# Kernel tuning notes

Hardware: AMD Instinct MI355X
Metric: run time of the kernel (lower is better)

The kernel has to match this reference:

```python
import jax, jax.numpy as jnp
import numpy as np

B, NB, BD, H = 524288, 8, 16, 64  # batch, n_bundles, bundle_dim, hidden_dim

def setup_inputs() -> dict:
    key = jax.random.key(0)
    ks = jax.random.split(key, 8)
    z = jax.random.normal(ks[0], (B, NB, BD), dtype=jnp.float32)
    w1 = jax.random.normal(ks[1], (H, NB), dtype=jnp.float32) * (1.0 / np.sqrt(NB))
    b1 = jnp.zeros((H,), dtype=jnp.float32)
    w2 = jax.random.normal(ks[2], (H, H), dtype=jnp.float32) * (1.0 / np.sqrt(H))
    b2 = jnp.zeros((H,), dtype=jnp.float32)
    w3 = jax.random.normal(ks[3], (NB, H), dtype=jnp.float32) * (1.0 / np.sqrt(H))
    mix_w = jax.random.normal(ks[4], (NB, NB, BD, BD), dtype=jnp.float32) * 0.01
    gate_bias = jnp.zeros((NB,), dtype=jnp.float32)
    return {"z": z, "w1": w1, "b1": b1, "w2": w2, "b2": b2, "w3": w3,
            "mix_w": mix_w, "gate_bias": gate_bias}

def reference(z, w1, b1, w2, b2, w3, mix_w, gate_bias):
    # per-bundle norms: [B, NB]
    norms = jnp.linalg.norm(z, axis=-1) + 1e-8
    # tiny gating MLP (exact GELU like torch nn.GELU default)
    h = jax.nn.gelu(norms @ w1.T + b1, approximate=False)
    h = jax.nn.gelu(h @ w2.T + b2, approximate=False)
    scales = jax.nn.softplus(h @ w3.T)                      # [B, NB]
    equivariant = z * scales[:, :, None]                    # [B, NB, BD]
    # cross-bundle mixing: mixing[b,i,k] = sum_{j,d} z[b,j,d] * W[i,j,k,d]
    mixing = jnp.einsum('bjd,ijkd->bik', z, mix_w)          # [B, NB, BD]
    gates = jax.nn.sigmoid(gate_bias)[None, :, None]        # [1, NB, 1]
    return z + (equivariant + gates * mixing)
```

## Files before the change

kernel.cpp:

```cpp
#include <hip/hip_runtime.h>
#include <hip/hip_fp16.h>

typedef __bf16   bf16x8 __attribute__((ext_vector_type(8)));
typedef _Float16 f16x8  __attribute__((ext_vector_type(8)));
typedef float    f32x4  __attribute__((ext_vector_type(4)));
typedef unsigned short ushort8 __attribute__((ext_vector_type(8)));

__device__ __forceinline__ unsigned short f2bf(float f){
  unsigned u = __builtin_bit_cast(unsigned, f);
  u = (u + 0x7FFFu + ((u >> 16) & 1u)) >> 16;
  return (unsigned short)u;
}

__device__ __forceinline__ float gelu_fast(float x){
  float u = 0.7978845608f * x * __builtin_fmaf(0.044715f, x * x, 1.0f);
  float e = __expf(2.0f * __builtin_fabsf(u));
  float t = __builtin_fmaf(-2.0f, __builtin_amdgcn_rcpf(e + 1.0f), 1.0f);
  t = __builtin_copysignf(t, u);
  return 0.5f * x * (1.0f + t);
}

__device__ __forceinline__ float softplus_fast(float x){
  float e = __expf(-__builtin_fabsf(x));
  return fmaxf(x, 0.0f) + __logf(1.0f + e);
}

__global__ void prepack_wt(const float* __restrict__ mix_w,
                           unsigned short* __restrict__ wt){
  int tid = blockIdx.x * 256 + threadIdx.x;
  int f = tid >> 6, L = tid & 63;
  int ks = f & 3, nt = f >> 2;
  int q = L >> 4, c = L & 15;
  int N = nt * 16 + c;
  int i = N >> 4, ko = N & 15;
  unsigned pk[4];
#pragma unroll
  for (int p = 0; p < 4; ++p){
    int K0 = ks * 32 + q * 8 + 2 * p;
    int K1 = K0 + 1;
    unsigned lo = f2bf(mix_w[((i*8 + (K0>>4))*16 + ko)*16 + (K0&15)]);
    unsigned hi = f2bf(mix_w[((i*8 + (K1>>4))*16 + ko)*16 + (K1&15)]);
    pk[p] = lo | (hi << 16);
  }
  uint4 v; v.x = pk[0]; v.y = pk[1]; v.z = pk[2]; v.w = pk[3];
  ((uint4*)wt)[tid] = v;
}

__global__ __launch_bounds__(256, 5)
void soft_eq_kernel(const float* __restrict__ z,
                    const float* __restrict__ w1,  const float* __restrict__ b1,
                    const float* __restrict__ w2,  const float* __restrict__ b2,
                    const float* __restrict__ w3,  const float* __restrict__ gate_bias,
                    const unsigned short* __restrict__ wt,
                    float* __restrict__ out){
  __shared__ __align__(16) _Float16 h1s[64 * 64];
  __shared__ __align__(16) _Float16 h2s[64 * 64];
  __shared__ float gatesS[8];
  float (*normsS)[8] = (float(*)[8])h2s;
  float (*scalesS)[9] = (float(*)[9])h1s;

  const int t = threadIdx.x;
  const size_t base = (size_t)blockIdx.x * (64 * 128);
  const float4* zg = (const float4*)(z + base);

#pragma unroll
  for (int it = 0; it < 8; ++it){
    int idx = t + it * 256;
    float4 v = zg[idx];
    int r  = idx >> 5;
    int bi = (idx & 31) >> 2;
    float ss = v.x*v.x + v.y*v.y + v.z*v.z + v.w*v.w;
    ss += __shfl_xor(ss, 1);
    ss += __shfl_xor(ss, 2);
    if ((t & 3) == 0) normsS[r][bi] = sqrtf(ss) + 1e-8f;
  }

  const int i = t & 63, rg = t >> 6;
  float w1r[8];
  { const float4* p = (const float4*)(w1 + i * 8);
    float4 a = p[0], bq = p[1];
    w1r[0]=a.x; w1r[1]=a.y; w1r[2]=a.z; w1r[3]=a.w;
    w1r[4]=bq.x; w1r[5]=bq.y; w1r[6]=bq.z; w1r[7]=bq.w; }
  const float b1r = b1[i];
  __syncthreads();

#pragma unroll
  for (int chunk = 0; chunk < 16; ++chunk){
    int r = chunk * 4 + rg;
    const float4* np = (const float4*)normsS[r];
    float4 n0 = np[0], n1 = np[1];
    float pre = b1r + n0.x*w1r[0] + n0.y*w1r[1] + n0.z*w1r[2] + n0.w*w1r[3]
                    + n1.x*w1r[4] + n1.y*w1r[5] + n1.z*w1r[6] + n1.w*w1r[7];
    int u = (i >> 3) ^ (r & 7);
    h1s[r * 64 + u * 8 + (i & 7)] = (_Float16)gelu_fast(pre);
  }
  __syncthreads();

  const int w = rg, L = t & 63, q = L >> 4, c = L & 15;
  const int am = w * 16 + c;

  f16x8 a2[2];
#pragma unroll
  for (int ks = 0; ks < 2; ++ks){
    int u = (ks * 4 + q) ^ (am & 7);
    a2[ks] = *(const f16x8*)&h1s[am * 64 + u * 8];
  }
#pragma unroll
  for (int nt = 0; nt < 4; ++nt){
    int n = nt * 16 + c;
    f32x4 acc2 = {};
#pragma unroll
    for (int ks = 0; ks < 2; ++ks){
      const float4* wp = (const float4*)(w2 + n * 64 + ks * 32 + q * 8);
      float4 v0 = wp[0], v1 = wp[1];
      f16x8 bf;
      bf[0]=(_Float16)v0.x; bf[1]=(_Float16)v0.y; bf[2]=(_Float16)v0.z; bf[3]=(_Float16)v0.w;
      bf[4]=(_Float16)v1.x; bf[5]=(_Float16)v1.y; bf[6]=(_Float16)v1.z; bf[7]=(_Float16)v1.w;
      acc2 = __builtin_amdgcn_mfma_f32_16x16x32_f16(a2[ks], bf, acc2, 0, 0, 0);
    }
    float b2v = b2[n];
#pragma unroll
    for (int rr = 0; rr < 4; ++rr){
      int row = w * 16 + q * 4 + rr;
      int uu = (n >> 3) ^ (row & 7);
      h2s[row * 64 + uu * 8 + (n & 7)] = (_Float16)gelu_fast(acc2[rr] + b2v);
    }
  }
  __syncthreads();

  {
    f16x8 a3[2];
#pragma unroll
    for (int ks = 0; ks < 2; ++ks){
      int u = (ks * 4 + q) ^ (am & 7);
      a3[ks] = *(const f16x8*)&h2s[am * 64 + u * 8];
    }
    int n3 = c & 7;
    f32x4 acc3 = {};
#pragma unroll
    for (int ks = 0; ks < 2; ++ks){
      const float4* wp = (const float4*)(w3 + n3 * 64 + ks * 32 + q * 8);
      float4 v0 = wp[0], v1 = wp[1];
      f16x8 bf;
      bf[0]=(_Float16)v0.x; bf[1]=(_Float16)v0.y; bf[2]=(_Float16)v0.z; bf[3]=(_Float16)v0.w;
      bf[4]=(_Float16)v1.x; bf[5]=(_Float16)v1.y; bf[6]=(_Float16)v1.z; bf[7]=(_Float16)v1.w;
      acc3 = __builtin_amdgcn_mfma_f32_16x16x32_f16(a3[ks], bf, acc3, 0, 0, 0);
    }
    if (c < 8){
#pragma unroll
      for (int rr = 0; rr < 4; ++rr){
        int row = w * 16 + q * 4 + rr;
        scalesS[row][c] = softplus_fast(acc3[rr]);
      }
    }
  }
  if (t < 8) gatesS[t] = __builtin_amdgcn_rcpf(1.0f + __expf(-gate_bias[t]));
  __syncthreads();

  f32x4 acc[8] = {};
  const uint4* wtf = (const uint4*)wt;
  const float* zp = z + base;
#pragma unroll
  for (int ks = 0; ks < 4; ++ks){
    int ak = ks * 32 + q * 8;
    const float4* ap = (const float4*)(zp + am * 128 + ak);
    float4 a0 = ap[0], a1 = ap[1];
    ushort8 au;
    au[0]=f2bf(a0.x); au[1]=f2bf(a0.y); au[2]=f2bf(a0.z); au[3]=f2bf(a0.w);
    au[4]=f2bf(a1.x); au[5]=f2bf(a1.y); au[6]=f2bf(a1.z); au[7]=f2bf(a1.w);
    bf16x8 af = __builtin_bit_cast(bf16x8, au);
#pragma unroll
    for (int n = 0; n < 8; ++n){
      uint4 bv = wtf[(n * 4 + ks) * 64 + L];
      bf16x8 bfr = __builtin_bit_cast(bf16x8, bv);
      acc[n] = __builtin_amdgcn_mfma_f32_16x16x32_bf16(af, bfr, acc[n], 0, 0, 0);
    }
  }

  float* op = out + base;
#pragma unroll
  for (int n = 0; n < 8; ++n){
    float gate = gatesS[n];
#pragma unroll
    for (int rr = 0; rr < 4; ++rr){
      int row = w * 16 + q * 4 + rr;
      int col = n * 16 + c;
      float zv = zp[row * 128 + col];
      float sc = scalesS[row][n];
      op[row * 128 + col] = __builtin_fmaf(zv, sc, __builtin_fmaf(gate, acc[n][rr], zv));
    }
  }
}

extern "C" void kernel_launch(void* const* d_in, const int* in_sizes, int n_in,
                              void* d_out, int out_size, void* d_ws, size_t ws_size,
                              hipStream_t stream){
  const float* z         = (const float*)d_in[0];
  const float* w1        = (const float*)d_in[1];
  const float* b1        = (const float*)d_in[2];
  const float* w2        = (const float*)d_in[3];
  const float* b2        = (const float*)d_in[4];
  const float* w3        = (const float*)d_in[5];
  const float* mix_w     = (const float*)d_in[6];
  const float* gate_bias = (const float*)d_in[7];
  float* out = (float*)d_out;
  unsigned short* wt = (unsigned short*)d_ws;

  int B = in_sizes[0] / 128;
  prepack_wt<<<8, 256, 0, stream>>>(mix_w, wt);
  soft_eq_kernel<<<B / 64, 256, 0, stream>>>(z, w1, b1, w2, b2, w3, gate_bias, wt, out);
}
```

Measured before the change: 575.7 us.

## Load z once into registers, stage output via LDS for coalesced stores, prepack MLP weights

Each thread now loads its z row fragment into registers once and reuses it for both the norm computation and the bf16 mixing MFMA, which is moved ahead of the gating MLP. The epilogue stages gate*mixing through LDS in two halves so that z re-reads and output writes become row-contiguous float4 accesses. A new prepack kernel converts w2 and w3 to fp16 in MFMA fragment layout, removing per-block conversion. The cost is higher register pressure (launch bounds lowered to 4 waves), extra barriers, and one more small launch.

```diff
diff --git a/kernel.cpp b/kernel.cpp
--- a/kernel.cpp
+++ b/kernel.cpp
@@ -24,6 +24,7 @@
   float e = __expf(-__builtin_fabsf(x));
   return fmaxf(x, 0.0f) + __logf(1.0f + e);
 }
+
 
 __global__ void prepack_wt(const float* __restrict__ mix_w,
                            unsigned short* __restrict__ wt){
@@ -46,48 +47,96 @@
   ((uint4*)wt)[tid] = v;
 }
 
-__global__ __launch_bounds__(256, 5)
+__global__ void prepack_mlp(const float* __restrict__ w2,
+                            const float* __restrict__ w3,
+                            unsigned short* __restrict__ ws){
+  int tid = blockIdx.x * 256 + threadIdx.x;
+  if (tid < 512){
+    int f = tid >> 6, L = tid & 63;
+    int nt = f >> 1, ks = f & 1, q = L >> 4, c = L & 15;
+    const float* s = w2 + (nt*16 + c)*64 + ks*32 + q*8;
+    f16x8 h;
+#pragma unroll
+    for (int j = 0; j < 8; ++j) h[j] = (_Float16)s[j];
+    ((f16x8*)(ws + 16384))[tid] = h;
+  } else if (tid < 640){
+    int u = tid - 512;
+    int ks = u >> 6, L = u & 63, q = L >> 4, c = L & 15;
+    const float* s = w3 + (c & 7)*64 + ks*32 + q*8;
+    f16x8 h;
+#pragma unroll
+    for (int j = 0; j < 8; ++j) h[j] = (_Float16)s[j];
+    ((f16x8*)(ws + 20480))[u] = h;
+  }
+}
+
+__global__ __launch_bounds__(256, 4)
 void soft_eq_kernel(const float* __restrict__ z,
                     const float* __restrict__ w1,  const float* __restrict__ b1,
                     const float* __restrict__ w2,  const float* __restrict__ b2,
                     const float* __restrict__ w3,  const float* __restrict__ gate_bias,
                     const unsigned short* __restrict__ wt,
                     float* __restrict__ out){
-  __shared__ __align__(16) _Float16 h1s[64 * 64];
-  __shared__ __align__(16) _Float16 h2s[64 * 64];
-  __shared__ float gatesS[8];
-  float (*normsS)[8] = (float(*)[8])h2s;
-  float (*scalesS)[9] = (float(*)[9])h1s;
+  __shared__ __align__(16) unsigned char smemU[17408 + 3104];
+  _Float16* h1s = (_Float16*)smemU;
+  _Float16* h2s = (_Float16*)(smemU + 8192);
+  float*    stageF = (float*)smemU;
+  float*    nsS = (float*)(smemU + 17408);
 
   const int t = threadIdx.x;
+  const int w = t >> 6, L = t & 63, q = L >> 4, c = L & 15;
   const size_t base = (size_t)blockIdx.x * (64 * 128);
-  const float4* zg = (const float4*)(z + base);
-
-#pragma unroll
-  for (int it = 0; it < 8; ++it){
-    int idx = t + it * 256;
-    float4 v = zg[idx];
-    int r  = idx >> 5;
-    int bi = (idx & 31) >> 2;
-    float ss = v.x*v.x + v.y*v.y + v.z*v.z + v.w*v.w;
-    ss += __shfl_xor(ss, 1);
-    ss += __shfl_xor(ss, 2);
-    if ((t & 3) == 0) normsS[r][bi] = sqrtf(ss) + 1e-8f;
-  }
-
-  const int i = t & 63, rg = t >> 6;
+  const float* zp = z + base;
+
+  const int zrow = w * 16 + c;
+  const float* zr0 = zp + zrow * 128;
+  float4 zr[8];
+#pragma unroll
+  for (int ks = 0; ks < 4; ++ks){
+    zr[2*ks]   = *(const float4*)(zr0 + ks*32 + q*8);
+    zr[2*ks+1] = *(const float4*)(zr0 + ks*32 + q*8 + 4);
+  }
+#pragma unroll
+  for (int ks = 0; ks < 4; ++ks){
+    float4 a = zr[2*ks], b = zr[2*ks+1];
+    float ss = a.x*a.x + a.y*a.y + a.z*a.z + a.w*a.w
+             + b.x*b.x + b.y*b.y + b.z*b.z + b.w*b.w;
+    ss += __shfl_xor(ss, 16);
+    if (!(L & 16))
+      nsS[zrow * 12 + 2*ks + (q >> 1)] = sqrtf(ss) + 1e-8f;
+  }
+
+  const int i = t & 63;
   float w1r[8];
   { const float4* p = (const float4*)(w1 + i * 8);
     float4 a = p[0], bq = p[1];
     w1r[0]=a.x; w1r[1]=a.y; w1r[2]=a.z; w1r[3]=a.w;
     w1r[4]=bq.x; w1r[5]=bq.y; w1r[6]=bq.z; w1r[7]=bq.w; }
   const float b1r = b1[i];
+
+  f32x4 acc[8] = {};
+  const uint4* wtf = (const uint4*)wt;
+#pragma unroll
+  for (int ks = 0; ks < 4; ++ks){
+    float4 a0 = zr[2*ks], a1 = zr[2*ks+1];
+    ushort8 au;
+    au[0]=f2bf(a0.x); au[1]=f2bf(a0.y); au[2]=f2bf(a0.z); au[3]=f2bf(a0.w);
+    au[4]=f2bf(a1.x); au[5]=f2bf(a1.y); au[6]=f2bf(a1.z); au[7]=f2bf(a1.w);
+    bf16x8 af = __builtin_bit_cast(bf16x8, au);
+#pragma unroll
+    for (int n = 0; n < 8; ++n){
+      uint4 bv = wtf[(n * 4 + ks) * 64 + L];
+      bf16x8 bfr = __builtin_bit_cast(bf16x8, bv);
+      acc[n] = __builtin_amdgcn_mfma_f32_16x16x32_bf16(af, bfr, acc[n], 0, 0, 0);
+    }
+  }
+
   __syncthreads();
 
 #pragma unroll
   for (int chunk = 0; chunk < 16; ++chunk){
-    int r = chunk * 4 + rg;
-    const float4* np = (const float4*)normsS[r];
+    int r = chunk * 4 + w;
+    const float4* np = (const float4*)&nsS[r * 12];
     float4 n0 = np[0], n1 = np[1];
     float pre = b1r + n0.x*w1r[0] + n0.y*w1r[1] + n0.z*w1r[2] + n0.w*w1r[3]
                     + n1.x*w1r[4] + n1.y*w1r[5] + n1.z*w1r[6] + n1.w*w1r[7];
@@ -96,9 +145,9 @@
   }
   __syncthreads();
 
-  const int w = rg, L = t & 63, q = L >> 4, c = L & 15;
   const int am = w * 16 + c;
 
+  const f16x8* w2f = (const f16x8*)(wt + 16384);
   f16x8 a2[2];
 #pragma unroll
   for (int ks = 0; ks < 2; ++ks){
@@ -110,14 +159,9 @@
     int n = nt * 16 + c;
     f32x4 acc2 = {};
 #pragma unroll
-    for (int ks = 0; ks < 2; ++ks){
-      const float4* wp = (const float4*)(w2 + n * 64 + ks * 32 + q * 8);
-      float4 v0 = wp[0], v1 = wp[1];
-      f16x8 bf;
-      bf[0]=(_Float16)v0.x; bf[1]=(_Float16)v0.y; bf[2]=(_Float16)v0.z; bf[3]=(_Float16)v0.w;
-      bf[4]=(_Float16)v1.x; bf[5]=(_Float16)v1.y; bf[6]=(_Float16)v1.z; bf[7]=(_Float16)v1.w;
-      acc2 = __builtin_amdgcn_mfma_f32_16x16x32_f16(a2[ks], bf, acc2, 0, 0, 0);
-    }
+    for (int ks = 0; ks < 2; ++ks)
+      acc2 = __builtin_amdgcn_mfma_f32_16x16x32_f16(a2[ks], w2f[(nt*2+ks)*64 + L],
+                                                    acc2, 0, 0, 0);
     float b2v = b2[n];
 #pragma unroll
     for (int rr = 0; rr < 4; ++rr){
@@ -129,66 +173,60 @@
   __syncthreads();
 
   {
+    const f16x8* w3f = (const f16x8*)(wt + 20480);
     f16x8 a3[2];
 #pragma unroll
     for (int ks = 0; ks < 2; ++ks){
       int u = (ks * 4 + q) ^ (am & 7);
       a3[ks] = *(const f16x8*)&h2s[am * 64 + u * 8];
     }
-    int n3 = c & 7;
     f32x4 acc3 = {};
 #pragma unroll
-    for (int ks = 0; ks < 2; ++ks){
-      const float4* wp = (const float4*)(w3 + n3 * 64 + ks * 32 + q * 8);
-      float4 v0 = wp[0], v1 = wp[1];
-      f16x8 bf;
-      bf[0]=(_Float16)v0.x; bf[1]=(_Float16)v0.y; bf[2]=(_Float16)v0.z; bf[3]=(_Float16)v0.w;
-      bf[4]=(_Float16)v1.x; bf[5]=(_Float16)v1.y; bf[6]=(_Float16)v1.z; bf[7]=(_Float16)v1.w;
-      acc3 = __builtin_amdgcn_mfma_f32_16x16x32_f16(a3[ks], bf, acc3, 0, 0, 0);
-    }
+    for (int ks = 0; ks < 2; ++ks)
+      acc3 = __builtin_amdgcn_mfma_f32_16x16x32_f16(a3[ks], w3f[ks*64 + L],
+                                                    acc3, 0, 0, 0);
     if (c < 8){
 #pragma unroll
       for (int rr = 0; rr < 4; ++rr){
         int row = w * 16 + q * 4 + rr;
-        scalesS[row][c] = softplus_fast(acc3[rr]);
+        nsS[row * 12 + c] = softplus_fast(acc3[rr]);
       }
     }
   }
-  if (t < 8) gatesS[t] = __builtin_amdgcn_rcpf(1.0f + __expf(-gate_bias[t]));
-  __syncthreads();
-
-  f32x4 acc[8] = {};
-  const uint4* wtf = (const uint4*)wt;
-  const float* zp = z + base;
-#pragma unroll
-  for (int ks = 0; ks < 4; ++ks){
-    int ak = ks * 32 + q * 8;
-    const float4* ap = (const float4*)(zp + am * 128 + ak);
-    float4 a0 = ap[0], a1 = ap[1];
-    ushort8 au;
-    au[0]=f2bf(a0.x); au[1]=f2bf(a0.y); au[2]=f2bf(a0.z); au[3]=f2bf(a0.w);
-    au[4]=f2bf(a1.x); au[5]=f2bf(a1.y); au[6]=f2bf(a1.z); au[7]=f2bf(a1.w);
-    bf16x8 af = __builtin_bit_cast(bf16x8, au);
-#pragma unroll
-    for (int n = 0; n < 8; ++n){
-      uint4 bv = wtf[(n * 4 + ks) * 64 + L];
-      bf16x8 bfr = __builtin_bit_cast(bf16x8, bv);
-      acc[n] = __builtin_amdgcn_mfma_f32_16x16x32_bf16(af, bfr, acc[n], 0, 0, 0);
-    }
-  }
+  if (t < 8) nsS[768 + t] = __builtin_amdgcn_rcpf(1.0f + __expf(-gate_bias[t]));
+  __syncthreads();
 
   float* op = out + base;
 #pragma unroll
-  for (int n = 0; n < 8; ++n){
-    float gate = gatesS[n];
-#pragma unroll
-    for (int rr = 0; rr < 4; ++rr){
-      int row = w * 16 + q * 4 + rr;
-      int col = n * 16 + c;
-      float zv = zp[row * 128 + col];
-      float sc = scalesS[row][n];
-      op[row * 128 + col] = __builtin_fmaf(zv, sc, __builtin_fmaf(gate, acc[n][rr], zv));
-    }
+  for (int half = 0; half < 2; ++half){
+#pragma unroll
+    for (int np = 0; np < 4; ++np){
+      int n = half * 4 + np;
+      float g = nsS[768 + n];
+#pragma unroll
+      for (int rr = 0; rr < 4; ++rr)
+        stageF[(w*16 + q*4 + rr) * 68 + np*16 + c] = g * acc[n][rr];
+    }
+    __syncthreads();
+    {
+      int row = t >> 2, cc = (t & 3) * 16;
+      float sc = nsS[row * 12 + half * 4 + (t & 3)];
+      const float4* zr4 = (const float4*)(zp + row * 128 + half * 64 + cc);
+      const float*  sp  = &stageF[row * 68 + cc];
+      float4*       or4 = (float4*)(op + row * 128 + half * 64 + cc);
+#pragma unroll
+      for (int k = 0; k < 4; ++k){
+        float4 zv = zr4[k];
+        float4 st = *(const float4*)(sp + k * 4);
+        float4 o;
+        o.x = __builtin_fmaf(zv.x, sc, zv.x + st.x);
+        o.y = __builtin_fmaf(zv.y, sc, zv.y + st.y);
+        o.z = __builtin_fmaf(zv.z, sc, zv.z + st.z);
+        o.w = __builtin_fmaf(zv.w, sc, zv.w + st.w);
+        or4[k] = o;
+      }
+    }
+    if (half == 0) __syncthreads();
   }
 }
 
@@ -208,5 +246,6 @@
 
   int B = in_sizes[0] / 128;
   prepack_wt<<<8, 256, 0, stream>>>(mix_w, wt);
+  prepack_mlp<<<3, 256, 0, stream>>>(w2, w3, wt);
   soft_eq_kernel<<<B / 64, 256, 0, stream>>>(z, w1, b1, w2, b2, w3, gate_bias, wt, out);
 }
```

Result: faster. 501.5 us (-12.9%).
